# Performance work log

Measured on AMD Instinct MI355X. Metric: run time of the kernel, lower is better.

Reference implementation:

```python
import jax, jax.numpy as jnp
import numpy as np

SCALE = 0.1    # BinarizeConv2dSDP scale factor
BN_EPS = 1e-5

def _binarize(x):
    # straight-through sign binarization (STE): forward = sign(x), grad = identity
    return x + jax.lax.stop_gradient(jnp.sign(x) - x)

def _bin_conv3x3(x, w, stride=1):
    # binarize activations and weights; per-output-channel weight scaling alpha = mean|w|
    a_b = _binarize(x)
    alpha = jnp.mean(jnp.abs(w), axis=(1, 2, 3))          # [Cout]
    w_b = _binarize(w)
    y = jax.lax.conv_general_dilated(
        a_b, w_b, window_strides=(stride, stride), padding=((1, 1), (1, 1)),
        dimension_numbers=('NCHW', 'OIHW', 'NCHW'))
    return y * (SCALE * alpha)[None, :, None, None]

def _batchnorm(x, gamma, beta):
    mu = jnp.mean(x, axis=(0, 2, 3), keepdims=True)
    var = jnp.var(x, axis=(0, 2, 3), keepdims=True)
    xh = (x - mu) * jax.lax.rsqrt(var + BN_EPS)
    return xh * gamma[None, :, None, None] + beta[None, :, None, None]

def _prelu(x, a):
    return jnp.where(x >= 0, x, a.reshape(()) * x)

def setup_inputs() -> dict:
    key = jax.random.key(0)
    ks = jax.random.split(key, 5)
    B, C, H, W = 64, 256, 28, 28
    return {
        'x': jax.random.normal(ks[0], (B, C, H, W), jnp.float32),
        'conv1_w': jax.random.normal(ks[1], (C, C, 3, 3), jnp.float32) * 0.05,
        'conv2_w': jax.random.normal(ks[2], (C, C, 3, 3), jnp.float32) * 0.05,
        'bn1_gamma': jnp.ones((C,), jnp.float32),
        'bn1_beta': jnp.zeros((C,), jnp.float32),
        'bn2_gamma': jnp.ones((C,), jnp.float32),
        'bn2_beta': jnp.zeros((C,), jnp.float32),
        'prelu1_a': jnp.full((1,), 0.25, jnp.float32),
        'prelu2_a': jnp.full((1,), 0.25, jnp.float32),
    }

def reference(x, conv1_w, conv2_w, bn1_gamma, bn1_beta, bn2_gamma, bn2_beta, prelu1_a, prelu2_a):
    residual = x
    out = _bin_conv3x3(x, conv1_w, stride=1)
    out = _batchnorm(out, bn1_gamma, bn1_beta)
    out = out + residual
    out = _prelu(out, prelu1_a)
    residual = out
    out = _bin_conv3x3(out, conv2_w, stride=1)
    out = _batchnorm(out, bn2_gamma, bn2_beta)
    out = out + residual
    out = _prelu(out, prelu2_a)
    return out
```

## Files before the change

kernel.cpp:

```cpp
#include <hip/hip_runtime.h>
#include <cstdint>

#define NB 64
#define NC 256
#define HW 784
#define NPIX (NB*HW)
#define NELEM ((size_t)NB*NC*HW)

#define MTILE 256
#define A_BYTES (314*256)
#define ZERO_OFF A_BYTES
#define W_OFF (A_BYTES + 256)
#define LDS_TOTAL (W_OFF + 2*32768)

typedef int v4i  __attribute__((ext_vector_type(4)));
typedef int v16i __attribute__((ext_vector_type(16)));

union U16 { signed char b[16]; int4 v; };

__global__ __launch_bounds__(256) void alpha_k(
    const float* __restrict__ w1, const float* __restrict__ w2,
    float* __restrict__ al1, float* __restrict__ al2) {
  int blk = blockIdx.x;
  int conv = blk >> 8, cout = blk & 255;
  const float* w = (conv ? w2 : w1) + (size_t)cout * 2304;
  int t = threadIdx.x;
  float s = 0.0f;
  for (int i = t; i < 2304; i += 256) s += fabsf(w[i]);
  __shared__ float red[256];
  red[t] = s;
  __syncthreads();
  for (int st = 128; st > 0; st >>= 1) {
    if (t < st) red[t] += red[t + st];
    __syncthreads();
  }
  if (t == 0) (conv ? al2 : al1)[cout] = red[0] / 2304.0f;
}

__global__ __launch_bounds__(256) void wfrag_k(
    const float* __restrict__ w1, const float* __restrict__ w2,
    signed char* __restrict__ Wf1, signed char* __restrict__ Wf2) {
  int bi = blockIdx.x;
  int conv = bi / 72, r = bi % 72, tap = r >> 3, cg = r & 7;
  const float* w = conv ? w2 : w1;
  signed char* Wf = conv ? Wf2 : Wf1;
  int t = threadIdx.x;
  for (int e = t; e < 512; e += 256) {
    int c = e >> 6, lane = e & 63;
    int cout = cg * 32 + (lane & 31);
    int cin0 = c * 32 + (lane >> 5) * 16;
    U16 u;
#pragma unroll
    for (int bb = 0; bb < 16; ++bb) {
      float v = w[((size_t)cout * 256 + cin0 + bb) * 9 + tap];
      u.b[bb] = v > 0.f ? 1 : (v < 0.f ? -1 : 0);
    }
    *(int4*)(Wf + ((((size_t)tap * 8 + c) * 8 + cg) * 64 + lane) * 16) = u.v;
  }
}

__global__ __launch_bounds__(256) void pack_x(
    const float* __restrict__ in, signed char* __restrict__ A) {
  __shared__ float tile[256 * 33];
  int t = threadIdx.x;
  int P0 = blockIdx.x * 32;
  int pl = t & 31, c0 = t >> 5;
  int P = P0 + pl;
  int b = P / HW, hw = P - b * HW;
  size_t base = (size_t)b * (NC * HW) + (size_t)c0 * HW + hw;
#pragma unroll
  for (int i = 0; i < 32; ++i)
    tile[(i * 8 + c0) * 33 + pl] = in[base + (size_t)i * 8 * HW];
  __syncthreads();
  int g = t >> 4, pls = t & 15;
#pragma unroll
  for (int ph = 0; ph < 2; ++ph) {
    int pp = ph * 16 + pls;
    U16 u;
#pragma unroll
    for (int bb = 0; bb < 16; ++bb) {
      float v = tile[(g * 16 + bb) * 33 + pp];
      u.b[bb] = v > 0.f ? 1 : (v < 0.f ? -1 : 0);
    }
    *(int4*)(A + (size_t)(P0 + pp) * 256 + g * 16) = u.v;
  }
}

__global__ __launch_bounds__(512, 2) void conv_mfma(
    const signed char* __restrict__ A, const signed char* __restrict__ Wf,
    short* __restrict__ dotb,
    int* __restrict__ pd, int* __restrict__ pq) {
  extern __shared__ signed char smem[];
  signed char* As = smem;
  signed char* Wlds = smem + W_OFF;

  int t = threadIdx.x;
  int lane = t & 63, wid = t >> 6;
  int mblk = blockIdx.x;
  int p0 = mblk * MTILE;
  int wm = wid & 3, wn = wid >> 2;
  int khalf = lane >> 5;

  {
    const signed char* src = A + (size_t)(p0 - 29) * 256;
#pragma unroll
    for (int i = 0; i < 10; ++i) {
      int off = i * 8192 + t * 16;
      if (off < A_BYTES) {
        int4 d = *(const int4*)(src + off);
        int r = off >> 8, g = (off >> 4) & 15;
        int gs = g ^ ((r + 3) & 15);
        *(int4*)(As + r * 256 + gs * 16) = d;
      }
    }
    if (t < 16) { int4 z = {0, 0, 0, 0}; *(int4*)(As + ZERO_OFF + t * 16) = z; }
  }
  {
#pragma unroll
    for (int k = 0; k < 4; ++k) {
      int4 d = *(const int4*)(Wf + k * 8192 + t * 16);
      *(int4*)(Wlds + k * 8192 + t * 16) = d;
    }
  }

  int prow[2], hh[2], ww[2];
#pragma unroll
  for (int i = 0; i < 2; ++i) {
    int p = p0 + wm * 64 + i * 32 + (lane & 31);
    prow[i] = p;
    int hw = p % HW;
    hh[i] = hw / 28;
    ww[i] = hw - hh[i] * 28;
  }
  __syncthreads();

  v16i acc[2][4];
#pragma unroll
  for (int i = 0; i < 2; ++i)
#pragma unroll
    for (int j = 0; j < 4; ++j) { v16i z = {0}; acc[i][j] = z; }

  int rbT[2], kkT[2];

#pragma unroll
  for (int ht = 0; ht < 18; ++ht) {
    const int cur = ht & 1;

    if ((ht & 1) == 0) {
      const int tap = ht >> 1;
      const int ky = tap / 3, kx = tap % 3;
      const int dlt = (ky - 1) * 28 + (kx - 1);
#pragma unroll
      for (int i = 0; i < 2; ++i) {
        int hp = hh[i] + ky - 1, wp = ww[i] + kx - 1;
        bool val = ((unsigned)hp < 28u) && ((unsigned)wp < 28u);
        int pr = prow[i] + dlt;
        rbT[i] = val ? (pr - (p0 - 29)) * 256 : ZERO_OFF;
        kkT[i] = val ? ((pr & 15) << 4) : 0;
      }
    }

    int4 wreg0, wreg1, wreg2, wreg3;
    if (ht < 17) {
      const signed char* wsrc = Wf + (size_t)(ht + 1) * 32768 + t * 16;
      wreg0 = *(const int4*)(wsrc);
      wreg1 = *(const int4*)(wsrc + 8192);
      wreg2 = *(const int4*)(wsrc + 16384);
      wreg3 = *(const int4*)(wsrc + 24576);
    }

#pragma unroll
    for (int c = 0; c < 4; ++c) {
      const int gch = (ht & 1) * 4 + c;
      v4i a0 = *(const v4i*)(As + rbT[0] + (((gch * 2 + khalf) << 4) ^ kkT[0]));
      v4i a1 = *(const v4i*)(As + rbT[1] + (((gch * 2 + khalf) << 4) ^ kkT[1]));
      const signed char* wb =
          Wlds + cur * 32768 + (c * 8 + wn * 4) * 1024 + lane * 16;
      v4i w0 = *(const v4i*)(wb);
      v4i w1 = *(const v4i*)(wb + 1024);
      v4i w2 = *(const v4i*)(wb + 2048);
      v4i w3 = *(const v4i*)(wb + 3072);
      acc[0][0] = __builtin_amdgcn_mfma_i32_32x32x32_i8(a0, w0, acc[0][0], 0, 0, 0);
      acc[0][1] = __builtin_amdgcn_mfma_i32_32x32x32_i8(a0, w1, acc[0][1], 0, 0, 0);
      acc[0][2] = __builtin_amdgcn_mfma_i32_32x32x32_i8(a0, w2, acc[0][2], 0, 0, 0);
      acc[0][3] = __builtin_amdgcn_mfma_i32_32x32x32_i8(a0, w3, acc[0][3], 0, 0, 0);
      acc[1][0] = __builtin_amdgcn_mfma_i32_32x32x32_i8(a1, w0, acc[1][0], 0, 0, 0);
      acc[1][1] = __builtin_amdgcn_mfma_i32_32x32x32_i8(a1, w1, acc[1][1], 0, 0, 0);
      acc[1][2] = __builtin_amdgcn_mfma_i32_32x32x32_i8(a1, w2, acc[1][2], 0, 0, 0);
      acc[1][3] = __builtin_amdgcn_mfma_i32_32x32x32_i8(a1, w3, acc[1][3], 0, 0, 0);
    }

    if (ht < 17) {
      signed char* wdst = Wlds + (cur ^ 1) * 32768 + t * 16;
      *(int4*)(wdst)         = wreg0;
      *(int4*)(wdst + 8192)  = wreg1;
      *(int4*)(wdst + 16384) = wreg2;
      *(int4*)(wdst + 24576) = wreg3;
      __syncthreads();
    }
  }

#pragma unroll
  for (int j = 0; j < 4; ++j) {
    int s = 0, sq = 0;
#pragma unroll
    for (int i = 0; i < 2; ++i)
#pragma unroll
      for (int q = 0; q < 16; ++q) {
        int v = acc[i][j][q];
        s += v; sq += v * v;
      }
    s += __shfl_xor(s, 32); sq += __shfl_xor(sq, 32);
    if (lane < 32) {
      int row = mblk * 4 + wm;
      int co = wn * 128 + j * 32 + lane;
      pd[row * 256 + co] = s;
      pq[row * 256 + co] = sq;
    }
  }

#pragma unroll
  for (int i = 0; i < 2; ++i) {
    int pr = p0 + wm * 64 + i * 32 + 4 * khalf;
#pragma unroll
    for (int j = 0; j < 4; ++j) {
      int cb = wn * 128 + j * 32;
#pragma unroll
      for (int q = 0; q < 16; ++q) {
        int row = pr + (q & 3) + 8 * (q >> 2);
        dotb[(size_t)row * 256 + cb + (lane & 31)] = (short)acc[i][j][q];
      }
    }
  }
}

__global__ __launch_bounds__(256) void bn_finalize(
    const int* __restrict__ pd, const int* __restrict__ pq,
    const float* __restrict__ alpha, const float* __restrict__ gamma,
    const float* __restrict__ beta, float* __restrict__ scale,
    float* __restrict__ shift) {
  int c = blockIdx.x, t = threadIdx.x;
  long long D = 0, D2 = 0;
  for (int r = t; r < 784; r += 256) {
    D  += (long long)pd[r * 256 + c];
    D2 += (long long)pq[r * 256 + c];
  }
  __shared__ long long rd[256], rq[256];
  rd[t] = D; rq[t] = D2;
  __syncthreads();
  for (int st = 128; st > 0; st >>= 1) {
    if (t < st) { rd[t] += rd[t + st]; rq[t] += rq[t + st]; }
    __syncthreads();
  }
  if (t == 0) {
    float sc = 0.1f * alpha[c];
    const float invN = 1.0f / (float)(NB * HW);
    float md  = (float)rd[0] * invN;
    float ex2 = (float)rq[0] * invN;
    float var = sc * sc * (ex2 - md * md);
    float rs = rsqrtf(var + 1e-5f);
    float g = gamma[c];
    scale[c] = rs * g * sc;
    shift[c] = beta[c] - sc * md * rs * g;
  }
}

__global__ __launch_bounds__(256) void bn_mid(
    const short* __restrict__ dot, const float* __restrict__ x,
    const float* __restrict__ scale, const float* __restrict__ shift,
    const float* __restrict__ pa, float* __restrict__ a1,
    signed char* __restrict__ A) {
  __shared__ short rawd[32 * 264];
  __shared__ float tile[256 * 33];
  __shared__ float ssc[256], ssh[256];
  int t = threadIdx.x;
  int P0 = blockIdx.x * 32;
  ssc[t] = scale[t]; ssh[t] = shift[t];
  float ap = pa[0];
#pragma unroll
  for (int i = 0; i < 4; ++i) {
    int idx = i * 256 + t;
    int pl = idx >> 5, g = idx & 31;
    int4 d = *(const int4*)(dot + (size_t)(P0 + pl) * 256 + g * 8);
    *(int4*)(&rawd[pl * 264 + g * 8]) = d;
  }
  __syncthreads();
  int pl = t & 31, c0 = t >> 5;
  int P = P0 + pl;
  int b = P / HW, hw = P - b * HW;
  size_t base = (size_t)b * (NC * HW) + (size_t)c0 * HW + hw;
#pragma unroll
  for (int i = 0; i < 32; ++i) {
    int c = i * 8 + c0;
    size_t addr = base + (size_t)i * 8 * HW;
    float d = (float)rawd[pl * 264 + c];
    float v = fmaf(d, ssc[c], ssh[c]) + x[addr];
    float o = v >= 0.0f ? v : ap * v;
    a1[addr] = o;
    tile[c * 33 + pl] = o;
  }
  __syncthreads();
  int g = t >> 4, pls = t & 15;
#pragma unroll
  for (int ph = 0; ph < 2; ++ph) {
    int pp = ph * 16 + pls;
    U16 u;
#pragma unroll
    for (int bb = 0; bb < 16; ++bb) {
      float v = tile[(g * 16 + bb) * 33 + pp];
      u.b[bb] = v > 0.f ? 1 : (v < 0.f ? -1 : 0);
    }
    *(int4*)(A + (size_t)(P0 + pp) * 256 + g * 16) = u.v;
  }
}

__global__ __launch_bounds__(256) void bn_fin_apply(
    const short* __restrict__ dot, const float* __restrict__ res,
    const float* __restrict__ scale, const float* __restrict__ shift,
    const float* __restrict__ pa, float* __restrict__ out) {
  __shared__ short rawd[32 * 264];
  __shared__ float ssc[256], ssh[256];
  int t = threadIdx.x;
  int P0 = blockIdx.x * 32;
  ssc[t] = scale[t]; ssh[t] = shift[t];
  float ap = pa[0];
#pragma unroll
  for (int i = 0; i < 4; ++i) {
    int idx = i * 256 + t;
    int pl = idx >> 5, g = idx & 31;
    int4 d = *(const int4*)(dot + (size_t)(P0 + pl) * 256 + g * 8);
    *(int4*)(&rawd[pl * 264 + g * 8]) = d;
  }
  __syncthreads();
  int pl = t & 31, c0 = t >> 5;
  int P = P0 + pl;
  int b = P / HW, hw = P - b * HW;
  size_t base = (size_t)b * (NC * HW) + (size_t)c0 * HW + hw;
#pragma unroll
  for (int i = 0; i < 32; ++i) {
    int c = i * 8 + c0;
    size_t addr = base + (size_t)i * 8 * HW;
    float d = (float)rawd[pl * 264 + c];
    float v = fmaf(d, ssc[c], ssh[c]) + res[addr];
    out[addr] = v >= 0.0f ? v : ap * v;
  }
}

extern "C" void kernel_launch(void* const* d_in, const int* in_sizes, int n_in,
                              void* d_out, int out_size, void* d_ws, size_t ws_size,
                              hipStream_t stream) {
  const float* x   = (const float*)d_in[0];
  const float* w1  = (const float*)d_in[1];
  const float* w2  = (const float*)d_in[2];
  const float* g1  = (const float*)d_in[3];
  const float* b1  = (const float*)d_in[4];
  const float* g2  = (const float*)d_in[5];
  const float* b2  = (const float*)d_in[6];
  const float* pa1 = (const float*)d_in[7];
  const float* pa2 = (const float*)d_in[8];
  float* out = (float*)d_out;

  char* ws = (char*)d_ws;
  short*       dotb = (short*)ws;       ws += (size_t)NPIX * 256 * 2;
  signed char* Abuf = (signed char*)ws; ws += (size_t)NPIX * 256;
  signed char* Wf1  = (signed char*)ws; ws += 589824;
  signed char* Wf2  = (signed char*)ws; ws += 589824;
  int* pd1 = (int*)ws; ws += 784 * 256 * 4;
  int* pq1 = (int*)ws; ws += 784 * 256 * 4;
  int* pd2 = (int*)ws; ws += 784 * 256 * 4;
  int* pq2 = (int*)ws; ws += 784 * 256 * 4;
  float* alpha1 = (float*)ws; ws += 1024;
  float* alpha2 = (float*)ws; ws += 1024;
  float* scale1 = (float*)ws; ws += 1024;
  float* shift1 = (float*)ws; ws += 1024;
  float* scale2 = (float*)ws; ws += 1024;
  float* shift2 = (float*)ws; ws += 1024;

  static int attr_done = 0;
  if (!attr_done) {
    hipFuncSetAttribute((const void*)conv_mfma,
                        hipFuncAttributeMaxDynamicSharedMemorySize, LDS_TOTAL);
    attr_done = 1;
  }

  alpha_k<<<512, 256, 0, stream>>>(w1, w2, alpha1, alpha2);
  wfrag_k<<<144, 256, 0, stream>>>(w1, w2, Wf1, Wf2);
  pack_x<<<NPIX / 32, 256, 0, stream>>>(x, Abuf);

  conv_mfma<<<196, 512, LDS_TOTAL, stream>>>(Abuf, Wf1, dotb, pd1, pq1);
  bn_finalize<<<256, 256, 0, stream>>>(pd1, pq1, alpha1, g1, b1, scale1, shift1);
  bn_mid<<<NPIX / 32, 256, 0, stream>>>(dotb, x, scale1, shift1, pa1, out, Abuf);

  conv_mfma<<<196, 512, LDS_TOTAL, stream>>>(Abuf, Wf2, dotb, pd2, pq2);
  bn_finalize<<<256, 256, 0, stream>>>(pd2, pq2, alpha2, g2, b2, scale2, shift2);
  bn_fin_apply<<<NPIX / 32, 256, 0, stream>>>(dotb, out, scale2, shift2, pa2, out);
}
```

Measured before the change: 164.1 us.

## Stream conv weights into LDS via direct global-to-LDS loads with split barriers

Weight tiles in the MFMA conv kernel are now copied straight from global memory into the double-buffered LDS with global_load_lds, prefetching two stages ahead and waiting with explicit vmcnt waits and raw barriers. This replaces the register-staged copy, removing VGPR pressure and the LDS store instructions. MFMA sections are also raised in wave priority. Separately, the intermediate activation now goes to a dedicated workspace buffer instead of aliasing the output, which adds a full-size tensor of extra workspace.

```diff
diff --git a/kernel.cpp b/kernel.cpp
--- a/kernel.cpp
+++ b/kernel.cpp
@@ -8,15 +8,24 @@
 #define NELEM ((size_t)NB*NC*HW)
 
 #define MTILE 256
-#define A_BYTES (314*256)
+#define HALO_ROWS 314
+#define A_BYTES (HALO_ROWS*256)
 #define ZERO_OFF A_BYTES
-#define W_OFF (A_BYTES + 256)
-#define LDS_TOTAL (W_OFF + 2*32768)
+#define W_LDS_OFF (A_BYTES + 256)
+#define W_BUF_SZ 32768
+#define CONV_LDS (W_LDS_OFF + 2*W_BUF_SZ)
 
 typedef int v4i  __attribute__((ext_vector_type(4)));
 typedef int v16i __attribute__((ext_vector_type(16)));
 
 union U16 { signed char b[16]; int4 v; };
+
+__device__ __forceinline__ void gload_lds16(const signed char* src,
+                                            signed char* dst) {
+  __builtin_amdgcn_global_load_lds(
+      (const __attribute__((address_space(1))) void*)src,
+      (__attribute__((address_space(3))) void*)dst, 16, 0, 0);
+}
 
 __global__ __launch_bounds__(256) void alpha_k(
     const float* __restrict__ w1, const float* __restrict__ w2,
@@ -92,7 +101,7 @@
     int* __restrict__ pd, int* __restrict__ pq) {
   extern __shared__ signed char smem[];
   signed char* As = smem;
-  signed char* Wlds = smem + W_OFF;
+  signed char* Wlds = smem + W_LDS_OFF;
 
   int t = threadIdx.x;
   int lane = t & 63, wid = t >> 6;
@@ -115,13 +124,6 @@
     }
     if (t < 16) { int4 z = {0, 0, 0, 0}; *(int4*)(As + ZERO_OFF + t * 16) = z; }
   }
-  {
-#pragma unroll
-    for (int k = 0; k < 4; ++k) {
-      int4 d = *(const int4*)(Wf + k * 8192 + t * 16);
-      *(int4*)(Wlds + k * 8192 + t * 16) = d;
-    }
-  }
 
   int prow[2], hh[2], ww[2];
 #pragma unroll
@@ -134,48 +136,55 @@
   }
   __syncthreads();
 
+#pragma unroll
+  for (int h = 0; h < 2; ++h) {
+    const signed char* wsrc = Wf + (size_t)h * W_BUF_SZ + wid * 4096 + lane * 16;
+    signed char* wdst = Wlds + h * W_BUF_SZ + wid * 4096;
+#pragma unroll
+    for (int j = 0; j < 4; ++j)
+      gload_lds16(wsrc + j * 1024, wdst + j * 1024);
+  }
+
   v16i acc[2][4];
 #pragma unroll
   for (int i = 0; i < 2; ++i)
 #pragma unroll
     for (int j = 0; j < 4; ++j) { v16i z = {0}; acc[i][j] = z; }
 
-  int rbT[2], kkT[2];
-
-#pragma unroll
-  for (int ht = 0; ht < 18; ++ht) {
-    const int cur = ht & 1;
-
-    if ((ht & 1) == 0) {
-      const int tap = ht >> 1;
-      const int ky = tap / 3, kx = tap % 3;
+  int rb0 = 0, rb1 = 0, kk0 = 0, kk1 = 0;
+
+#pragma unroll
+  for (int h = 0; h < 18; ++h) {
+    if (h < 17) asm volatile("s_waitcnt vmcnt(4)" ::: "memory");
+    else        asm volatile("s_waitcnt vmcnt(0)" ::: "memory");
+    __builtin_amdgcn_s_barrier();
+
+    if ((h & 1) == 0) {
+      const int tap = h >> 1;
+      const int ky = (tap >= 3) + (tap >= 6);
+      const int kx = tap - 3 * ky;
       const int dlt = (ky - 1) * 28 + (kx - 1);
-#pragma unroll
-      for (int i = 0; i < 2; ++i) {
-        int hp = hh[i] + ky - 1, wp = ww[i] + kx - 1;
-        bool val = ((unsigned)hp < 28u) && ((unsigned)wp < 28u);
-        int pr = prow[i] + dlt;
-        rbT[i] = val ? (pr - (p0 - 29)) * 256 : ZERO_OFF;
-        kkT[i] = val ? ((pr & 15) << 4) : 0;
-      }
-    }
-
-    int4 wreg0, wreg1, wreg2, wreg3;
-    if (ht < 17) {
-      const signed char* wsrc = Wf + (size_t)(ht + 1) * 32768 + t * 16;
-      wreg0 = *(const int4*)(wsrc);
-      wreg1 = *(const int4*)(wsrc + 8192);
-      wreg2 = *(const int4*)(wsrc + 16384);
-      wreg3 = *(const int4*)(wsrc + 24576);
-    }
-
-#pragma unroll
-    for (int c = 0; c < 4; ++c) {
-      const int gch = (ht & 1) * 4 + c;
-      v4i a0 = *(const v4i*)(As + rbT[0] + (((gch * 2 + khalf) << 4) ^ kkT[0]));
-      v4i a1 = *(const v4i*)(As + rbT[1] + (((gch * 2 + khalf) << 4) ^ kkT[1]));
-      const signed char* wb =
-          Wlds + cur * 32768 + (c * 8 + wn * 4) * 1024 + lane * 16;
+      int hp = hh[0] + ky - 1, wp = ww[0] + kx - 1;
+      bool val = ((unsigned)hp < 28u) && ((unsigned)wp < 28u);
+      int pr = prow[0] + dlt;
+      rb0 = val ? (pr - (p0 - 29)) * 256 : ZERO_OFF;
+      kk0 = val ? ((pr & 15) << 4) : 0;
+      hp = hh[1] + ky - 1; wp = ww[1] + kx - 1;
+      val = ((unsigned)hp < 28u) && ((unsigned)wp < 28u);
+      pr = prow[1] + dlt;
+      rb1 = val ? (pr - (p0 - 29)) * 256 : ZERO_OFF;
+      kk1 = val ? ((pr & 15) << 4) : 0;
+    }
+
+    const signed char* wbuf = Wlds + (h & 1) * W_BUF_SZ;
+    __builtin_amdgcn_s_setprio(1);
+#pragma unroll
+    for (int cl = 0; cl < 4; ++cl) {
+      const int chunk = (h & 1) * 4 + cl;
+      const int gl4 = ((chunk * 2 + khalf) << 4);
+      v4i a0 = *(const v4i*)(As + rb0 + (gl4 ^ kk0));
+      v4i a1 = *(const v4i*)(As + rb1 + (gl4 ^ kk1));
+      const signed char* wb = wbuf + cl * 8192 + wn * 4096 + lane * 16;
       v4i w0 = *(const v4i*)(wb);
       v4i w1 = *(const v4i*)(wb + 1024);
       v4i w2 = *(const v4i*)(wb + 2048);
@@ -189,14 +198,16 @@
       acc[1][2] = __builtin_amdgcn_mfma_i32_32x32x32_i8(a1, w2, acc[1][2], 0, 0, 0);
       acc[1][3] = __builtin_amdgcn_mfma_i32_32x32x32_i8(a1, w3, acc[1][3], 0, 0, 0);
     }
-
-    if (ht < 17) {
-      signed char* wdst = Wlds + (cur ^ 1) * 32768 + t * 16;
-      *(int4*)(wdst)         = wreg0;
-      *(int4*)(wdst + 8192)  = wreg1;
-      *(int4*)(wdst + 16384) = wreg2;
-      *(int4*)(wdst + 24576) = wreg3;
-      __syncthreads();
+    __builtin_amdgcn_s_setprio(0);
+    __builtin_amdgcn_s_barrier();
+
+    if (h + 2 < 18) {
+      const signed char* wsrc =
+          Wf + (size_t)(h + 2) * W_BUF_SZ + wid * 4096 + lane * 16;
+      signed char* wdst = Wlds + (h & 1) * W_BUF_SZ + wid * 4096;
+#pragma unroll
+      for (int j = 0; j < 4; ++j)
+        gload_lds16(wsrc + j * 1024, wdst + j * 1024);
     }
   }
 
@@ -365,6 +376,7 @@
   signed char* Abuf = (signed char*)ws; ws += (size_t)NPIX * 256;
   signed char* Wf1  = (signed char*)ws; ws += 589824;
   signed char* Wf2  = (signed char*)ws; ws += 589824;
+  float*       a1   = (float*)ws;       ws += NELEM * 4;
   int* pd1 = (int*)ws; ws += 784 * 256 * 4;
   int* pq1 = (int*)ws; ws += 784 * 256 * 4;
   int* pd2 = (int*)ws; ws += 784 * 256 * 4;
@@ -379,7 +391,7 @@
   static int attr_done = 0;
   if (!attr_done) {
     hipFuncSetAttribute((const void*)conv_mfma,
-                        hipFuncAttributeMaxDynamicSharedMemorySize, LDS_TOTAL);
+                        hipFuncAttributeMaxDynamicSharedMemorySize, CONV_LDS);
     attr_done = 1;
   }
 
@@ -387,11 +399,11 @@
   wfrag_k<<<144, 256, 0, stream>>>(w1, w2, Wf1, Wf2);
   pack_x<<<NPIX / 32, 256, 0, stream>>>(x, Abuf);
 
-  conv_mfma<<<196, 512, LDS_TOTAL, stream>>>(Abuf, Wf1, dotb, pd1, pq1);
+  conv_mfma<<<196, 512, CONV_LDS, stream>>>(Abuf, Wf1, dotb, pd1, pq1);
   bn_finalize<<<256, 256, 0, stream>>>(pd1, pq1, alpha1, g1, b1, scale1, shift1);
-  bn_mid<<<NPIX / 32, 256, 0, stream>>>(dotb, x, scale1, shift1, pa1, out, Abuf);
-
-  conv_mfma<<<196, 512, LDS_TOTAL, stream>>>(Abuf, Wf2, dotb, pd2, pq2);
+  bn_mid<<<NPIX / 32, 256, 0, stream>>>(dotb, x, scale1, shift1, pa1, a1, Abuf);
+
+  conv_mfma<<<196, 512, CONV_LDS, stream>>>(Abuf, Wf2, dotb, pd2, pq2);
   bn_finalize<<<256, 256, 0, stream>>>(pd2, pq2, alpha2, g2, b2, scale2, shift2);
-  bn_fin_apply<<<NPIX / 32, 256, 0, stream>>>(dotb, out, scale2, shift2, pa2, out);
-}
+  bn_fin_apply<<<NPIX / 32, 256, 0, stream>>>(dotb, a1, scale2, shift2, pa2, out);
+}
```

Result: faster. 158.0 us (-3.7%).
